# Performance work log

Hardware: AMD Instinct MI355X
Metric: run time of the kernel (lower is better)

Reference implementation:

```python
import jax, jax.numpy as jnp
import numpy as np

N_NODES = 100000
N_EDGES = 200000
Z_DIM = 64
ATTR_DIM = 768
HID = 128
N_CLASSES = 5


def setup_inputs() -> dict:
    key = jax.random.key(0)
    ks = jax.random.split(key, 6)
    z = jax.random.normal(ks[0], (N_NODES, Z_DIM), dtype=jnp.float32)
    edge_index = jax.random.randint(ks[1], (2, N_EDGES), 0, N_NODES, dtype=jnp.int64)
    edge_attr = jax.random.normal(ks[2], (N_EDGES, ATTR_DIM), dtype=jnp.float32)
    W1 = jax.random.normal(ks[3], (ATTR_DIM + Z_DIM, HID), dtype=jnp.float32) * 0.02
    b1 = jnp.zeros((HID,), dtype=jnp.float32)
    W2 = jax.random.normal(ks[4], (HID, N_CLASSES), dtype=jnp.float32) * 0.02
    b2 = jnp.zeros((N_CLASSES,), dtype=jnp.float32)
    return {"z": z, "edge_index": edge_index, "edge_attr": edge_attr,
            "W1": W1, "b1": b1, "W2": W2, "b2": b2}


def reference(z, edge_index, edge_attr, W1, b1, W2, b2):
    # decode(): gather endpoint embeddings, elementwise product  [E, 64]
    node_rep = z[edge_index[0]] * z[edge_index[1]]
    # concat with edge attributes -> [E, 64 + 768] (torch cat order: node_rep first)
    joint = jnp.concatenate([node_rep, edge_attr], axis=-1)
    # 2-layer MLP + softmax
    h = jax.nn.relu(joint @ W1 + b1)
    logits = h @ W2 + b2
    return jax.nn.softmax(logits, axis=-1)
```

## Files before the change

kernel.cpp:

```cpp
#include <hip/hip_runtime.h>
#include <hip/hip_bf16.h>

#define E_TOT 200000
#define NZ 64
#define ATTR_D 768
#define KD 832
#define HID_D 128
#define NCLS 5

typedef __attribute__((ext_vector_type(8))) short short8;
typedef __attribute__((ext_vector_type(4))) float f32x4;

__device__ __forceinline__ unsigned pk2(float a, float b) {
    __hip_bfloat162 h = __float22bfloat162_rn(make_float2(a, b));
    return *reinterpret_cast<unsigned*>(&h);
}

__global__ void prep_w1t(const float* __restrict__ W1, __hip_bfloat16* __restrict__ w1t) {
    int idx = blockIdx.x * 256 + threadIdx.x;
    if (idx >= HID_D * KD) return;
    int n = idx / KD;
    int k = idx - n * KD;
    w1t[idx] = __float2bfloat16(W1[(size_t)k * HID_D + n]);
}

__global__ __launch_bounds__(256) void gcn_main(
    const float* __restrict__ z, const int* __restrict__ ei,
    const float* __restrict__ attr, const __hip_bfloat16* __restrict__ w1t,
    const float* __restrict__ b1, const float* __restrict__ W2,
    const float* __restrict__ b2, float* __restrict__ out) {

    __shared__ uint4 As4[128 * 4];
    __shared__ uint4 Bs4[128 * 4];

    const int t  = threadIdx.x;
    const int e0 = blockIdx.x * 128;

    const int r    = t >> 1;
    const int half = t & 1;
    const int e    = e0 + r;
    const bool ev  = (e < E_TOT);
    int si = 0, di = 0;
    if (ev) { si = ei[e]; di = ei[E_TOT + e]; }
    const float4* zs = reinterpret_cast<const float4*>(z + (size_t)si * NZ);
    const float4* zd = reinterpret_cast<const float4*>(z + (size_t)di * NZ);
    const float4* ar = reinterpret_cast<const float4*>(attr + (size_t)e * ATTR_D);
    const uint4* wrow = reinterpret_cast<const uint4*>(w1t + r * KD);

    const int swz = (r >> 1) & 3;
    const int wc0 = half * 2;

    const int wv   = t >> 6;
    const int lane = t & 63;
    const int g    = lane >> 4;
    const int c0   = lane & 15;

    f32x4 acc[2][8];
#pragma unroll
    for (int m = 0; m < 2; ++m)
#pragma unroll
        for (int f = 0; f < 8; ++f) acc[m][f] = (f32x4){0.f, 0.f, 0.f, 0.f};

    for (int kt = 0; kt < 26; ++kt) {
        const int k0 = kt * 32;

        {
            const uint4* p = wrow + (k0 >> 3) + half * 2;
            uint4 q0 = p[0];
            uint4 q1 = p[1];
            Bs4[(r << 2) + (wc0 ^ swz)]       = q0;
            Bs4[(r << 2) + ((wc0 + 1) ^ swz)] = q1;
        }
        {
            float4 x0, x1, x2, x3;
            if (kt < 2) {
                int fo = (k0 + half * 16) >> 2;
                if (ev) {
                    float4 s0 = zs[fo], s1 = zs[fo + 1], s2 = zs[fo + 2], s3 = zs[fo + 3];
                    float4 d0 = zd[fo], d1 = zd[fo + 1], d2 = zd[fo + 2], d3 = zd[fo + 3];
                    x0 = make_float4(s0.x * d0.x, s0.y * d0.y, s0.z * d0.z, s0.w * d0.w);
                    x1 = make_float4(s1.x * d1.x, s1.y * d1.y, s1.z * d1.z, s1.w * d1.w);
                    x2 = make_float4(s2.x * d2.x, s2.y * d2.y, s2.z * d2.z, s2.w * d2.w);
                    x3 = make_float4(s3.x * d3.x, s3.y * d3.y, s3.z * d3.z, s3.w * d3.w);
                } else {
                    x0 = x1 = x2 = x3 = make_float4(0.f, 0.f, 0.f, 0.f);
                }
            } else {
                int fo = (k0 - 64 + half * 16) >> 2;
                if (ev) {
                    x0 = ar[fo]; x1 = ar[fo + 1]; x2 = ar[fo + 2]; x3 = ar[fo + 3];
                } else {
                    x0 = x1 = x2 = x3 = make_float4(0.f, 0.f, 0.f, 0.f);
                }
            }
            uint4 q0, q1;
            q0.x = pk2(x0.x, x0.y); q0.y = pk2(x0.z, x0.w);
            q0.z = pk2(x1.x, x1.y); q0.w = pk2(x1.z, x1.w);
            q1.x = pk2(x2.x, x2.y); q1.y = pk2(x2.z, x2.w);
            q1.z = pk2(x3.x, x3.y); q1.w = pk2(x3.z, x3.w);
            As4[(r << 2) + (wc0 ^ swz)]       = q0;
            As4[(r << 2) + ((wc0 + 1) ^ swz)] = q1;
        }
        __syncthreads();

        {
            int row0 = wv * 32 + c0;
            int row1 = row0 + 16;
            short8 a0 = *reinterpret_cast<const short8*>(&As4[(row0 << 2) + (g ^ ((row0 >> 1) & 3))]);
            short8 a1 = *reinterpret_cast<const short8*>(&As4[(row1 << 2) + (g ^ ((row1 >> 1) & 3))]);
            short8 bf[8];
#pragma unroll
            for (int f = 0; f < 8; ++f) {
                int n = f * 16 + c0;
                bf[f] = *reinterpret_cast<const short8*>(&Bs4[(n << 2) + (g ^ ((n >> 1) & 3))]);
            }
#pragma unroll
            for (int f = 0; f < 8; ++f) {
                acc[0][f] = __builtin_amdgcn_mfma_f32_16x16x32_bf16(a0, bf[f], acc[0][f], 0, 0, 0);
                acc[1][f] = __builtin_amdgcn_mfma_f32_16x16x32_bf16(a1, bf[f], acc[1][f], 0, 0, 0);
            }
        }
        __syncthreads();
    }

    float b1v[8], w2v[8][NCLS];
#pragma unroll
    for (int f = 0; f < 8; ++f) {
        int col = f * 16 + c0;
        b1v[f] = b1[col];
#pragma unroll
        for (int cc = 0; cc < NCLS; ++cc) w2v[f][cc] = W2[col * NCLS + cc];
    }
    float b2v[NCLS];
#pragma unroll
    for (int cc = 0; cc < NCLS; ++cc) b2v[cc] = b2[cc];

#pragma unroll
    for (int m = 0; m < 2; ++m) {
#pragma unroll
        for (int i = 0; i < 4; ++i) {
            float lg[NCLS] = {0.f, 0.f, 0.f, 0.f, 0.f};
#pragma unroll
            for (int f = 0; f < 8; ++f) {
                float h = acc[m][f][i] + b1v[f];
                h = fmaxf(h, 0.f);
#pragma unroll
                for (int cc = 0; cc < NCLS; ++cc) lg[cc] = fmaf(h, w2v[f][cc], lg[cc]);
            }
#pragma unroll
            for (int mask = 1; mask < 16; mask <<= 1) {
#pragma unroll
                for (int cc = 0; cc < NCLS; ++cc) lg[cc] += __shfl_xor(lg[cc], mask);
            }
#pragma unroll
            for (int cc = 0; cc < NCLS; ++cc) lg[cc] += b2v[cc];

            float mx = fmaxf(fmaxf(fmaxf(lg[0], lg[1]), fmaxf(lg[2], lg[3])), lg[4]);
            float q[NCLS];
            float s = 0.f;
#pragma unroll
            for (int cc = 0; cc < NCLS; ++cc) { q[cc] = __expf(lg[cc] - mx); s += q[cc]; }
            float inv = 1.0f / s;
            float num = (c0 == 0) ? q[0] : (c0 == 1) ? q[1] : (c0 == 2) ? q[2]
                      : (c0 == 3) ? q[3] : q[4];
            int rowl = wv * 32 + m * 16 + g * 4 + i;
            int eo = e0 + rowl;
            if (eo < E_TOT && c0 < NCLS) out[(size_t)eo * NCLS + c0] = num * inv;
        }
    }
}

extern "C" void kernel_launch(void* const* d_in, const int* in_sizes, int n_in,
                              void* d_out, int out_size, void* d_ws, size_t ws_size,
                              hipStream_t stream) {
    const float* z    = (const float*)d_in[0];
    const int*   ei   = (const int*)d_in[1];
    const float* attr = (const float*)d_in[2];
    const float* W1   = (const float*)d_in[3];
    const float* b1   = (const float*)d_in[4];
    const float* W2   = (const float*)d_in[5];
    const float* b2   = (const float*)d_in[6];
    float* out = (float*)d_out;
    __hip_bfloat16* w1t = (__hip_bfloat16*)d_ws;

    prep_w1t<<<(HID_D * KD + 255) / 256, 256, 0, stream>>>(W1, w1t);
    const int nblk = (E_TOT + 127) / 128;
    gcn_main<<<nblk, 256, 0, stream>>>(z, ei, attr, w1t, b1, W2, b2, out);
}
```

Baseline: 216.2 us.

## Load MFMA operands straight from global into registers with double buffering

Drops the shared-memory staging of A and B tiles and both __syncthreads per K step. Each lane now loads its MFMA fragments of attr/z and the transposed bf16 W1 directly from global memory, with two register sets so the loads for step k+1 are in flight while step k runs its MFMAs. Launch bounds request two blocks per SM. The cost is a higher register count and redundant W1 loads from every wave, which will mostly hit cache. Out-of-range edges are clamped to the last edge instead of zero-filled, and their stores stay masked.

Measured after the change: 294.4 us. 1.36x slower.

```diff
diff --git a/kernel.cpp b/kernel.cpp
--- a/kernel.cpp
+++ b/kernel.cpp
@@ -7,6 +7,7 @@
 #define KD 832
 #define HID_D 128
 #define NCLS 5
+#define NKT 26
 
 typedef __attribute__((ext_vector_type(8))) short short8;
 typedef __attribute__((ext_vector_type(4))) float f32x4;
@@ -14,6 +15,15 @@
 __device__ __forceinline__ unsigned pk2(float a, float b) {
     __hip_bfloat162 h = __float22bfloat162_rn(make_float2(a, b));
     return *reinterpret_cast<unsigned*>(&h);
+}
+
+__device__ __forceinline__ short8 pack8(const float4 x0, const float4 x1) {
+    union { unsigned u[4]; short8 s; } r;
+    r.u[0] = pk2(x0.x, x0.y);
+    r.u[1] = pk2(x0.z, x0.w);
+    r.u[2] = pk2(x1.x, x1.y);
+    r.u[3] = pk2(x1.z, x1.w);
+    return r.s;
 }
 
 __global__ void prep_w1t(const float* __restrict__ W1, __hip_bfloat16* __restrict__ w1t) {
@@ -24,36 +34,61 @@
     w1t[idx] = __float2bfloat16(W1[(size_t)k * HID_D + n]);
 }
 
-__global__ __launch_bounds__(256) void gcn_main(
+__global__ __launch_bounds__(256, 2) void gcn_main(
     const float* __restrict__ z, const int* __restrict__ ei,
     const float* __restrict__ attr, const __hip_bfloat16* __restrict__ w1t,
     const float* __restrict__ b1, const float* __restrict__ W2,
     const float* __restrict__ b2, float* __restrict__ out) {
 
-    __shared__ uint4 As4[128 * 4];
-    __shared__ uint4 Bs4[128 * 4];
-
-    const int t  = threadIdx.x;
-    const int e0 = blockIdx.x * 128;
-
-    const int r    = t >> 1;
-    const int half = t & 1;
-    const int e    = e0 + r;
-    const bool ev  = (e < E_TOT);
-    int si = 0, di = 0;
-    if (ev) { si = ei[e]; di = ei[E_TOT + e]; }
-    const float4* zs = reinterpret_cast<const float4*>(z + (size_t)si * NZ);
-    const float4* zd = reinterpret_cast<const float4*>(z + (size_t)di * NZ);
-    const float4* ar = reinterpret_cast<const float4*>(attr + (size_t)e * ATTR_D);
-    const uint4* wrow = reinterpret_cast<const uint4*>(w1t + r * KD);
-
-    const int swz = (r >> 1) & 3;
-    const int wc0 = half * 2;
-
+    const int t    = threadIdx.x;
     const int wv   = t >> 6;
     const int lane = t & 63;
     const int g    = lane >> 4;
     const int c0   = lane & 15;
+    const int e0   = blockIdx.x * 128;
+
+    const float* ab[2];
+    const float* zs[2];
+    const float* zd[2];
+#pragma unroll
+    for (int m = 0; m < 2; ++m) {
+        int e  = e0 + wv * 32 + m * 16 + c0;
+        int ec = e < E_TOT ? e : E_TOT - 1;
+        ab[m] = attr + (size_t)ec * ATTR_D + g * 8;
+        int si = ei[ec];
+        int di = ei[E_TOT + ec];
+        zs[m] = z + (size_t)si * NZ + g * 8;
+        zd[m] = z + (size_t)di * NZ + g * 8;
+    }
+    const __hip_bfloat16* wbase = w1t + (size_t)c0 * KD + g * 8;
+
+    auto LOADB = [&](int kt, short8 (&b)[8]) {
+#pragma unroll
+        for (int f = 0; f < 8; ++f)
+            b[f] = *reinterpret_cast<const short8*>(wbase + f * 16 * KD + kt * 32);
+    };
+    auto LOADA = [&](int kt, float4 (&ar)[2][2]) {
+        if (kt >= 2) {
+            const int off = kt * 32 - NZ;
+#pragma unroll
+            for (int m = 0; m < 2; ++m) {
+                const float4* p = reinterpret_cast<const float4*>(ab[m] + off);
+                ar[m][0] = p[0];
+                ar[m][1] = p[1];
+            }
+        } else {
+            const int off = kt * 32;
+#pragma unroll
+            for (int m = 0; m < 2; ++m) {
+                const float4* ps = reinterpret_cast<const float4*>(zs[m] + off);
+                const float4* pd = reinterpret_cast<const float4*>(zd[m] + off);
+                float4 s0 = ps[0], s1 = ps[1];
+                float4 d0 = pd[0], d1 = pd[1];
+                ar[m][0] = make_float4(s0.x * d0.x, s0.y * d0.y, s0.z * d0.z, s0.w * d0.w);
+                ar[m][1] = make_float4(s1.x * d1.x, s1.y * d1.y, s1.z * d1.z, s1.w * d1.w);
+            }
+        }
+    };
 
     f32x4 acc[2][8];
 #pragma unroll
@@ -61,66 +96,36 @@
 #pragma unroll
         for (int f = 0; f < 8; ++f) acc[m][f] = (f32x4){0.f, 0.f, 0.f, 0.f};
 
-    for (int kt = 0; kt < 26; ++kt) {
-        const int k0 = kt * 32;
+    float4 arA[2][2], arB[2][2];
+    short8 bA[8], bB[8];
+    LOADB(0, bA);
+    LOADA(0, arA);
 
+    for (int kt = 0; kt < NKT; kt += 2) {
+        LOADB(kt + 1, bB);
+        LOADA(kt + 1, arB);
         {
-            const uint4* p = wrow + (k0 >> 3) + half * 2;
-            uint4 q0 = p[0];
-            uint4 q1 = p[1];
-            Bs4[(r << 2) + (wc0 ^ swz)]       = q0;
-            Bs4[(r << 2) + ((wc0 + 1) ^ swz)] = q1;
+            short8 a0 = pack8(arA[0][0], arA[0][1]);
+            short8 a1 = pack8(arA[1][0], arA[1][1]);
+#pragma unroll
+            for (int f = 0; f < 8; ++f) {
+                acc[0][f] = __builtin_amdgcn_mfma_f32_16x16x32_bf16(a0, bA[f], acc[0][f], 0, 0, 0);
+                acc[1][f] = __builtin_amdgcn_mfma_f32_16x16x32_bf16(a1, bA[f], acc[1][f], 0, 0, 0);
+            }
+        }
+        if (kt + 2 < NKT) {
+            LOADB(kt + 2, bA);
+            LOADA(kt + 2, arA);
         }
         {
-            float4 x0, x1, x2, x3;
-            if (kt < 2) {
-                int fo = (k0 + half * 16) >> 2;
-                if (ev) {
-                    float4 s0 = zs[fo], s1 = zs[fo + 1], s2 = zs[fo + 2], s3 = zs[fo + 3];
-                    float4 d0 = zd[fo], d1 = zd[fo + 1], d2 = zd[fo + 2], d3 = zd[fo + 3];
-                    x0 = make_float4(s0.x * d0.x, s0.y * d0.y, s0.z * d0.z, s0.w * d0.w);
-                    x1 = make_float4(s1.x * d1.x, s1.y * d1.y, s1.z * d1.z, s1.w * d1.w);
-                    x2 = make_float4(s2.x * d2.x, s2.y * d2.y, s2.z * d2.z, s2.w * d2.w);
-                    x3 = make_float4(s3.x * d3.x, s3.y * d3.y, s3.z * d3.z, s3.w * d3.w);
-                } else {
-                    x0 = x1 = x2 = x3 = make_float4(0.f, 0.f, 0.f, 0.f);
-                }
-            } else {
-                int fo = (k0 - 64 + half * 16) >> 2;
-                if (ev) {
-                    x0 = ar[fo]; x1 = ar[fo + 1]; x2 = ar[fo + 2]; x3 = ar[fo + 3];
-                } else {
-                    x0 = x1 = x2 = x3 = make_float4(0.f, 0.f, 0.f, 0.f);
-                }
-            }
-            uint4 q0, q1;
-            q0.x = pk2(x0.x, x0.y); q0.y = pk2(x0.z, x0.w);
-            q0.z = pk2(x1.x, x1.y); q0.w = pk2(x1.z, x1.w);
-            q1.x = pk2(x2.x, x2.y); q1.y = pk2(x2.z, x2.w);
-            q1.z = pk2(x3.x, x3.y); q1.w = pk2(x3.z, x3.w);
-            As4[(r << 2) + (wc0 ^ swz)]       = q0;
-            As4[(r << 2) + ((wc0 + 1) ^ swz)] = q1;
-        }
-        __syncthreads();
-
-        {
-            int row0 = wv * 32 + c0;
-            int row1 = row0 + 16;
-            short8 a0 = *reinterpret_cast<const short8*>(&As4[(row0 << 2) + (g ^ ((row0 >> 1) & 3))]);
-            short8 a1 = *reinterpret_cast<const short8*>(&As4[(row1 << 2) + (g ^ ((row1 >> 1) & 3))]);
-            short8 bf[8];
+            short8 a0 = pack8(arB[0][0], arB[0][1]);
+            short8 a1 = pack8(arB[1][0], arB[1][1]);
 #pragma unroll
             for (int f = 0; f < 8; ++f) {
-                int n = f * 16 + c0;
-                bf[f] = *reinterpret_cast<const short8*>(&Bs4[(n << 2) + (g ^ ((n >> 1) & 3))]);
-            }
-#pragma unroll
-            for (int f = 0; f < 8; ++f) {
-                acc[0][f] = __builtin_amdgcn_mfma_f32_16x16x32_bf16(a0, bf[f], acc[0][f], 0, 0, 0);
-                acc[1][f] = __builtin_amdgcn_mfma_f32_16x16x32_bf16(a1, bf[f], acc[1][f], 0, 0, 0);
+                acc[0][f] = __builtin_amdgcn_mfma_f32_16x16x32_bf16(a0, bB[f], acc[0][f], 0, 0, 0);
+                acc[1][f] = __builtin_amdgcn_mfma_f32_16x16x32_bf16(a1, bB[f], acc[1][f], 0, 0, 0);
             }
         }
-        __syncthreads();
     }
 
     float b1v[8], w2v[8][NCLS];
```
